# Kernel optimization log

Hardware: AMD Instinct MI355X
Metric: run time of the kernel (lower is better)

The kernel has to match this reference:

```python
import jax, jax.numpy as jnp
import numpy as np

N_NODES = 100000
N_EDGES = 1_000_000
NODE_DIM = 64
EDGE_DIM = 32
HIDDEN = 64


def _unif(key, shape, fan_in):
    bound = 1.0 / np.sqrt(fan_in)
    return jax.random.uniform(key, shape, jnp.float32, -bound, bound)


def setup_inputs() -> dict:
    key = jax.random.key(0)
    ks = jax.random.split(key, 11)
    node_features = jax.random.normal(ks[0], (N_NODES, NODE_DIM), jnp.float32)
    edge_index = jax.random.randint(ks[1], (2, N_EDGES), 0, N_NODES, dtype=jnp.int64)
    edge_features = jax.random.normal(ks[2], (N_EDGES, EDGE_DIM), jnp.float32)
    in_dim = 2 * NODE_DIM + EDGE_DIM
    # message MLP: Linear(in_dim, HIDDEN) -> ReLU -> Linear(HIDDEN, HIDDEN)
    W1 = _unif(ks[3], (HIDDEN, in_dim), in_dim)
    b1 = _unif(ks[4], (HIDDEN,), in_dim)
    W2 = _unif(ks[5], (HIDDEN, HIDDEN), HIDDEN)
    b2 = _unif(ks[6], (HIDDEN,), HIDDEN)
    # GRUCell(input=HIDDEN, hidden=NODE_DIM); gates stacked [r; z; n]
    w_ih = _unif(ks[7], (3 * NODE_DIM, HIDDEN), NODE_DIM)
    w_hh = _unif(ks[8], (3 * NODE_DIM, NODE_DIM), NODE_DIM)
    b_ih = _unif(ks[9], (3 * NODE_DIM,), NODE_DIM)
    b_hh = _unif(ks[10], (3 * NODE_DIM,), NODE_DIM)
    return {
        "node_features": node_features,
        "edge_index": edge_index,
        "edge_features": edge_features,
        "W1": W1, "b1": b1, "W2": W2, "b2": b2,
        "w_ih": w_ih, "w_hh": w_hh, "b_ih": b_ih, "b_hh": b_hh,
    }


def reference(node_features, edge_index, edge_features, W1, b1, W2, b2, w_ih, w_hh, b_ih, b_hh):
    src, dst = edge_index[0], edge_index[1]
    # gather endpoints and build message MLP input: [E, 2*node_dim+edge_dim]
    x = jnp.concatenate([node_features[src], node_features[dst], edge_features], axis=-1)
    h = jax.nn.relu(x @ W1.T + b1)
    messages = h @ W2.T + b2  # [E, HIDDEN]
    # scatter-add into per-node aggregates
    agg = jax.ops.segment_sum(messages, dst, num_segments=node_features.shape[0])
    # GRUCell(agg, node_features) with torch gate order [r, z, n]
    gi = agg @ w_ih.T + b_ih
    gh = node_features @ w_hh.T + b_hh
    i_r, i_z, i_n = jnp.split(gi, 3, axis=-1)
    h_r, h_z, h_n = jnp.split(gh, 3, axis=-1)
    r = jax.nn.sigmoid(i_r + h_r)
    z = jax.nn.sigmoid(i_z + h_z)
    n = jnp.tanh(i_n + r * h_n)
    return (1.0 - z) * n + z * node_features
```

## Files before the change

kernel.cpp:

```cpp
#include <hip/hip_runtime.h>
#include <hip/hip_bf16.h>

#define N_NODES 100000
#define N_EDGES 1000000
#define CAP 64
#define OVF_CAP 65536

typedef __bf16 bf16x8 __attribute__((ext_vector_type(8)));
typedef float  f32x4  __attribute__((ext_vector_type(4)));

#define MFMA(a, b, c) __builtin_amdgcn_mfma_f32_16x16x32_bf16((a), (b), (c), 0, 0, 0)

__device__ __forceinline__ float sigmoid_f(float x) { return 1.f / (1.f + __expf(-x)); }
__device__ __forceinline__ float tanh_f(float x) {
    float cx = fminf(fmaxf(x, -30.f), 30.f);
    float e = __expf(-2.f * cx);
    return (1.f - e) / (1.f + e);
}

__global__ __launch_bounds__(256) void pq_kernel(
    const float* __restrict__ nf, const float* __restrict__ W1,
    const float* __restrict__ b1,
    __bf16* __restrict__ Pb, __bf16* __restrict__ Qb)
{
    const int lane = threadIdx.x & 63;
    const int r = lane & 15, g = lane >> 4;

    bf16x8 Bs[4][2], Bd[4][2];
    #pragma unroll
    for (int nt = 0; nt < 4; ++nt)
        #pragma unroll
        for (int kk = 0; kk < 2; ++kk) {
            const float* ws = &W1[(nt * 16 + r) * 160 + kk * 32 + g * 8];
            const float* wd = ws + 64;
            f32x4 s0 = *(const f32x4*)ws, s1 = *(const f32x4*)(ws + 4);
            f32x4 d0 = *(const f32x4*)wd, d1 = *(const f32x4*)(wd + 4);
            #pragma unroll
            for (int j = 0; j < 4; ++j) {
                Bs[nt][kk][j] = (__bf16)s0[j]; Bs[nt][kk][j + 4] = (__bf16)s1[j];
                Bd[nt][kk][j] = (__bf16)d0[j]; Bd[nt][kk][j + 4] = (__bf16)d1[j];
            }
        }
    float b1v[4];
    #pragma unroll
    for (int nt = 0; nt < 4; ++nt) b1v[nt] = b1[nt * 16 + r];

    const int wid = blockIdx.x * (blockDim.x >> 6) + (threadIdx.x >> 6);
    const int nW  = gridDim.x * (blockDim.x >> 6);
    for (int t = wid; t < N_NODES / 16; t += nW) {
        const int base = t * 16;
        bf16x8 A[2];
        #pragma unroll
        for (int kk = 0; kk < 2; ++kk) {
            const float* p = &nf[(size_t)(base + r) * 64 + kk * 32 + g * 8];
            f32x4 v0 = *(const f32x4*)p, v1 = *(const f32x4*)(p + 4);
            #pragma unroll
            for (int j = 0; j < 4; ++j) { A[kk][j] = (__bf16)v0[j]; A[kk][j + 4] = (__bf16)v1[j]; }
        }
        f32x4 accP[4] = {}, accQ[4] = {};
        #pragma unroll
        for (int nt = 0; nt < 4; ++nt)
            #pragma unroll
            for (int kk = 0; kk < 2; ++kk) {
                accP[nt] = MFMA(A[kk], Bs[nt][kk], accP[nt]);
                accQ[nt] = MFMA(A[kk], Bd[nt][kk], accQ[nt]);
            }
        #pragma unroll
        for (int nt = 0; nt < 4; ++nt)
            #pragma unroll
            for (int rr = 0; rr < 4; ++rr) {
                const int node = base + g * 4 + rr;
                const int col  = nt * 16 + r;
                Pb[(size_t)node * 64 + col] = (__bf16)(accP[nt][rr] + b1v[nt]);
                Qb[(size_t)node * 64 + col] = (__bf16)accQ[nt][rr];
            }
    }
}

__global__ __launch_bounds__(256) void e_kernel(
    const float* __restrict__ ef, const float* __restrict__ W1,
    __bf16* __restrict__ Eb)
{
    const int lane = threadIdx.x & 63;
    const int r = lane & 15, g = lane >> 4;

    bf16x8 Be[4];
    #pragma unroll
    for (int nt = 0; nt < 4; ++nt) {
        const float* w = &W1[(nt * 16 + r) * 160 + 128 + g * 8];
        f32x4 w0 = *(const f32x4*)w, w1 = *(const f32x4*)(w + 4);
        #pragma unroll
        for (int j = 0; j < 4; ++j) { Be[nt][j] = (__bf16)w0[j]; Be[nt][j + 4] = (__bf16)w1[j]; }
    }

    const int wid = blockIdx.x * (blockDim.x >> 6) + (threadIdx.x >> 6);
    const int nW  = gridDim.x * (blockDim.x >> 6);
    for (int t = wid; t < N_EDGES / 16; t += nW) {
        const int base = t * 16;
        bf16x8 Ae;
        {
            const float* p = &ef[(size_t)(base + r) * 32 + g * 8];
            f32x4 v0 = *(const f32x4*)p, v1 = *(const f32x4*)(p + 4);
            #pragma unroll
            for (int j = 0; j < 4; ++j) { Ae[j] = (__bf16)v0[j]; Ae[j + 4] = (__bf16)v1[j]; }
        }
        f32x4 accT[4] = {};
        #pragma unroll
        for (int nt = 0; nt < 4; ++nt) accT[nt] = MFMA(Ae, Be[nt], accT[nt]);
        #pragma unroll
        for (int nt = 0; nt < 4; ++nt)
            #pragma unroll
            for (int rr = 0; rr < 4; ++rr)
                Eb[(size_t)(base + g * 4 + rr) * 64 + nt * 16 + r] = (__bf16)accT[nt][rr];
    }
}

__global__ __launch_bounds__(256) void scatter_kernel(
    const int* __restrict__ ei, int* __restrict__ cnt,
    int2* __restrict__ slots, int* __restrict__ ovf)
{
    const int* srcI = ei;
    const int* dstI = ei + N_EDGES;
    int* ovfCnt = cnt + N_NODES;
    for (int e = blockIdx.x * blockDim.x + threadIdx.x; e < N_EDGES;
         e += gridDim.x * blockDim.x) {
        int d = dstI[e];
        int r = atomicAdd(&cnt[d], 1);
        if (r < CAP) slots[(size_t)d * CAP + r] = make_int2(e, srcI[e]);
        else { int o = atomicAdd(ovfCnt, 1); if (o < OVF_CAP) ovf[o] = e; }
    }
}

__global__ __launch_bounds__(256) void gather_kernel(
    const int* __restrict__ cnt, const int2* __restrict__ slots,
    const __bf16* __restrict__ Eb, const __bf16* __restrict__ Pb,
    const __bf16* __restrict__ Qb, float* __restrict__ Hsum)
{
    const int lane = threadIdx.x & 63;
    const int wid = blockIdx.x * (blockDim.x >> 6) + (threadIdx.x >> 6);
    const int nW  = gridDim.x * (blockDim.x >> 6);
    for (int n = wid; n < N_NODES; n += nW) {
        const int c = cnt[n];
        const int m = min(c, CAP);
        int2 sl = slots[(size_t)n * CAP + lane];
        float q = (float)Qb[(size_t)n * 64 + lane];
        float acc = 0.f;
        float ev = 0.f, pv = 0.f;
        if (m > 0) {
            int e0 = __shfl(sl.x, 0), s0 = __shfl(sl.y, 0);
            ev = (float)Eb[(size_t)e0 * 64 + lane];
            pv = (float)Pb[(size_t)s0 * 64 + lane];
        }
        for (int it = 0; it < m; ++it) {
            float ce = ev, cp = pv;
            if (it + 1 < m) {
                int e1 = __shfl(sl.x, it + 1), s1 = __shfl(sl.y, it + 1);
                ev = (float)Eb[(size_t)e1 * 64 + lane];
                pv = (float)Pb[(size_t)s1 * 64 + lane];
            }
            acc += fmaxf(ce + cp + q, 0.f);
        }
        Hsum[(size_t)n * 64 + lane] = acc;
    }
}

__global__ void ovf_kernel(
    const int* __restrict__ cnt, const int* __restrict__ ovf,
    const int* __restrict__ ei,
    const __bf16* __restrict__ Eb, const __bf16* __restrict__ Pb,
    const __bf16* __restrict__ Qb, float* __restrict__ Hsum)
{
    const int lane = threadIdx.x;
    int nv = min(cnt[N_NODES], OVF_CAP);
    const int* srcI = ei;
    const int* dstI = ei + N_EDGES;
    for (int i = blockIdx.x; i < nv; i += gridDim.x) {
        int e = ovf[i];
        int d = dstI[e], s = srcI[e];
        float v = fmaxf((float)Eb[(size_t)e * 64 + lane] +
                        (float)Pb[(size_t)s * 64 + lane] +
                        (float)Qb[(size_t)d * 64 + lane], 0.f);
        atomicAdd(&Hsum[(size_t)d * 64 + lane], v);
    }
}

__global__ __launch_bounds__(256) void prep_kernel(
    const float* __restrict__ w_ih, const float* __restrict__ W2,
    const float* __restrict__ b2, float* __restrict__ M, float* __restrict__ b2i)
{
    int tid = blockIdx.x * blockDim.x + threadIdx.x;
    if (tid < 192 * 64) {
        int d = tid >> 6, k = tid & 63;
        float s = 0.f;
        #pragma unroll 8
        for (int j = 0; j < 64; ++j) s += w_ih[d * 64 + j] * W2[j * 64 + k];
        M[tid] = s;
    }
    if (tid < 192) {
        float s = 0.f;
        for (int j = 0; j < 64; ++j) s += w_ih[tid * 64 + j] * b2[j];
        b2i[tid] = s;
    }
}

__global__ __launch_bounds__(256) void gru_kernel(
    const float* __restrict__ nf, const float* __restrict__ Hsum,
    const float* __restrict__ M, const float* __restrict__ w_hh,
    const float* __restrict__ b_ih, const float* __restrict__ b_hh,
    const float* __restrict__ b2i, const int* __restrict__ cnt,
    float* __restrict__ out)
{
    const int lane = threadIdx.x & 63;
    const int r = lane & 15, g = lane >> 4;
    const int wid = blockIdx.x * (blockDim.x >> 6) + (threadIdx.x >> 6);
    const int nW  = gridDim.x * (blockDim.x >> 6);

    float br[4], bz[4], bin_[4], bhn_[4];
    float c2r[4], c2z[4], c2n[4];
    #pragma unroll
    for (int nt = 0; nt < 4; ++nt) {
        const int d = nt * 16 + r;
        br[nt]   = b_ih[d] + b_hh[d];
        bz[nt]   = b_ih[64 + d] + b_hh[64 + d];
        bin_[nt] = b_ih[128 + d];
        bhn_[nt] = b_hh[128 + d];
        c2r[nt] = b2i ? b2i[d] : 0.f;
        c2z[nt] = b2i ? b2i[64 + d] : 0.f;
        c2n[nt] = b2i ? b2i[128 + d] : 0.f;
    }

    for (int t = wid; t < N_NODES / 16; t += nW) {
        const int base = t * 16;
        bf16x8 aaH[2], aaL[2], ahH[2], ahL[2];
        #pragma unroll
        for (int kk = 0; kk < 2; ++kk) {
            const float* pa = &Hsum[(size_t)(base + r) * 64 + kk * 32 + g * 8];
            const float* ph = &nf  [(size_t)(base + r) * 64 + kk * 32 + g * 8];
            f32x4 a0 = *(const f32x4*)pa, a1 = *(const f32x4*)(pa + 4);
            f32x4 h0 = *(const f32x4*)ph, h1 = *(const f32x4*)(ph + 4);
            #pragma unroll
            for (int j = 0; j < 4; ++j) {
                float av0 = a0[j], av1 = a1[j], hv0 = h0[j], hv1 = h1[j];
                __bf16 x;
                x = (__bf16)av0; aaH[kk][j]     = x; aaL[kk][j]     = (__bf16)(av0 - (float)x);
                x = (__bf16)av1; aaH[kk][j + 4] = x; aaL[kk][j + 4] = (__bf16)(av1 - (float)x);
                x = (__bf16)hv0; ahH[kk][j]     = x; ahL[kk][j]     = (__bf16)(hv0 - (float)x);
                x = (__bf16)hv1; ahH[kk][j + 4] = x; ahL[kk][j + 4] = (__bf16)(hv1 - (float)x);
            }
        }

        f32x4 accR[4] = {}, accZ[4] = {}, accIN[4] = {}, accHN[4] = {};
        #pragma unroll
        for (int c = 0; c < 3; ++c) {
            bf16x8 Bi[4][2], Bh[4][2];
            #pragma unroll
            for (int nt = 0; nt < 4; ++nt)
                #pragma unroll
                for (int kk = 0; kk < 2; ++kk) {
                    const float* wi = &M   [(size_t)(c * 64 + nt * 16 + r) * 64 + kk * 32 + g * 8];
                    const float* wh = &w_hh[(size_t)(c * 64 + nt * 16 + r) * 64 + kk * 32 + g * 8];
                    f32x4 i0 = *(const f32x4*)wi, i1 = *(const f32x4*)(wi + 4);
                    f32x4 h0 = *(const f32x4*)wh, h1 = *(const f32x4*)(wh + 4);
                    #pragma unroll
                    for (int j = 0; j < 4; ++j) {
                        Bi[nt][kk][j] = (__bf16)i0[j]; Bi[nt][kk][j + 4] = (__bf16)i1[j];
                        Bh[nt][kk][j] = (__bf16)h0[j]; Bh[nt][kk][j + 4] = (__bf16)h1[j];
                    }
                }
            #pragma unroll
            for (int nt = 0; nt < 4; ++nt) {
                f32x4 ai = {}, ah = {};
                #pragma unroll
                for (int kk = 0; kk < 2; ++kk) {
                    ai = MFMA(aaH[kk], Bi[nt][kk], ai);
                    ai = MFMA(aaL[kk], Bi[nt][kk], ai);
                    ah = MFMA(ahH[kk], Bh[nt][kk], ah);
                    ah = MFMA(ahL[kk], Bh[nt][kk], ah);
                }
                if (c == 0)      accR[nt] = ai + ah;
                else if (c == 1) accZ[nt] = ai + ah;
                else             { accIN[nt] = ai; accHN[nt] = ah; }
            }
        }
        #pragma unroll
        for (int nt = 0; nt < 4; ++nt)
            #pragma unroll
            for (int rr = 0; rr < 4; ++rr) {
                const int node = base + g * 4 + rr;
                const int d    = nt * 16 + r;
                float dg = cnt ? (float)cnt[node] : 0.f;
                float rg = sigmoid_f(accR[nt][rr] + br[nt] + dg * c2r[nt]);
                float zg = sigmoid_f(accZ[nt][rr] + bz[nt] + dg * c2z[nt]);
                float ng = tanh_f(accIN[nt][rr] + bin_[nt] + dg * c2n[nt] +
                                  rg * (accHN[nt][rr] + bhn_[nt]));
                float hv = nf[(size_t)node * 64 + d];
                out[(size_t)node * 64 + d] = (1.f - zg) * ng + zg * hv;
            }
    }
}

#define LDH 68
__global__ __launch_bounds__(256) void edge_kernel_fb(
    const int* __restrict__ ei, const float* __restrict__ ef,
    const float* __restrict__ W1, const float* __restrict__ W2,
    const float* __restrict__ b2,
    const __bf16* __restrict__ Pb, const __bf16* __restrict__ Qb,
    float* __restrict__ agg)
{
    __shared__ float lds_h[4][16 * LDH];
    const int lane = threadIdx.x & 63;
    const int r = lane & 15, g = lane >> 4;
    float* hb = lds_h[threadIdx.x >> 6];
    const int* srcI = ei;
    const int* dstI = ei + N_EDGES;

    bf16x8 Be[4];
    #pragma unroll
    for (int nt = 0; nt < 4; ++nt) {
        const float* w = &W1[(nt * 16 + r) * 160 + 128 + g * 8];
        f32x4 w0 = *(const f32x4*)w, w1 = *(const f32x4*)(w + 4);
        #pragma unroll
        for (int j = 0; j < 4; ++j) { Be[nt][j] = (__bf16)w0[j]; Be[nt][j + 4] = (__bf16)w1[j]; }
    }
    bf16x8 B2[4][2];
    #pragma unroll
    for (int nt = 0; nt < 4; ++nt)
        #pragma unroll
        for (int kk = 0; kk < 2; ++kk) {
            const float* w = &W2[(nt * 16 + r) * 64 + kk * 32 + g * 8];
            f32x4 w0 = *(const f32x4*)w, w1 = *(const f32x4*)(w + 4);
            #pragma unroll
            for (int j = 0; j < 4; ++j) { B2[nt][kk][j] = (__bf16)w0[j]; B2[nt][kk][j + 4] = (__bf16)w1[j]; }
        }
    float b2v[4];
    #pragma unroll
    for (int nt = 0; nt < 4; ++nt) b2v[nt] = b2[nt * 16 + r];

    const int wid = blockIdx.x * (blockDim.x >> 6) + (threadIdx.x >> 6);
    const int nW  = gridDim.x * (blockDim.x >> 6);
    for (int t = wid; t < N_EDGES / 16; t += nW) {
        const int base = t * 16;
        const int er = base + r;
        const int es = srcI[er], ed = dstI[er];
        bf16x8 Ae;
        {
            const float* p = &ef[(size_t)er * 32 + g * 8];
            f32x4 v0 = *(const f32x4*)p, v1 = *(const f32x4*)(p + 4);
            #pragma unroll
            for (int j = 0; j < 4; ++j) { Ae[j] = (__bf16)v0[j]; Ae[j + 4] = (__bf16)v1[j]; }
        }
        f32x4 accT[4] = {};
        #pragma unroll
        for (int nt = 0; nt < 4; ++nt) accT[nt] = MFMA(Ae, Be[nt], accT[nt]);
        #pragma unroll
        for (int nt = 0; nt < 4; ++nt)
            #pragma unroll
            for (int rr = 0; rr < 4; ++rr)
                hb[(g * 4 + rr) * LDH + nt * 16 + r] = accT[nt][rr];
        bf16x8 A2[2];
        #pragma unroll
        for (int kk = 0; kk < 2; ++kk) {
            const int k = kk * 32 + g * 8;
            const float* hp = &hb[r * LDH + k];
            f32x4 h0 = *(const f32x4*)hp, h1 = *(const f32x4*)(hp + 4);
            bf16x8 p8 = *(const bf16x8*)(Pb + (size_t)es * 64 + k);
            bf16x8 q8 = *(const bf16x8*)(Qb + (size_t)ed * 64 + k);
            #pragma unroll
            for (int j = 0; j < 4; ++j) {
                A2[kk][j]     = (__bf16)fmaxf(h0[j] + (float)p8[j]     + (float)q8[j],     0.f);
                A2[kk][j + 4] = (__bf16)fmaxf(h1[j] + (float)p8[j + 4] + (float)q8[j + 4], 0.f);
            }
        }
        f32x4 accM[4] = {};
        #pragma unroll
        for (int nt = 0; nt < 4; ++nt)
            #pragma unroll
            for (int kk = 0; kk < 2; ++kk)
                accM[nt] = MFMA(A2[kk], B2[nt][kk], accM[nt]);
        int4 d4 = *(const int4*)(dstI + base + g * 4);
        const int* dd = (const int*)&d4;
        #pragma unroll
        for (int rr = 0; rr < 4; ++rr) {
            float* dp = agg + (size_t)dd[rr] * 64;
            #pragma unroll
            for (int nt = 0; nt < 4; ++nt)
                atomicAdd(dp + nt * 16 + r, accM[nt][rr] + b2v[nt]);
        }
    }
}

extern "C" void kernel_launch(void* const* d_in, const int* in_sizes, int n_in,
                              void* d_out, int out_size, void* d_ws, size_t ws_size,
                              hipStream_t stream) {
    const float* nf  = (const float*)d_in[0];
    const int*   ei  = (const int*)  d_in[1];
    const float* ef  = (const float*)d_in[2];
    const float* W1  = (const float*)d_in[3];
    const float* b1  = (const float*)d_in[4];
    const float* W2  = (const float*)d_in[5];
    const float* b2  = (const float*)d_in[6];
    const float* wih = (const float*)d_in[7];
    const float* whh = (const float*)d_in[8];
    const float* bih = (const float*)d_in[9];
    const float* bhh = (const float*)d_in[10];
    float* out = (float*)d_out;

    char* ws = (char*)d_ws;
    size_t off = 0;
    auto alloc = [&](size_t bytes) { char* p = ws + off; off = (off + bytes + 255) & ~(size_t)255; return p; };
    int*    cnt   = (int*)   alloc((size_t)(N_NODES + 1) * 4);
    int*    ovf   = (int*)   alloc((size_t)OVF_CAP * 4);
    int2*   slots = (int2*)  alloc((size_t)N_NODES * CAP * 8);
    __bf16* Eb    = (__bf16*)alloc((size_t)N_EDGES * 64 * 2);
    __bf16* Pb    = (__bf16*)alloc((size_t)N_NODES * 64 * 2);
    __bf16* Qb    = (__bf16*)alloc((size_t)N_NODES * 64 * 2);
    float*  Hsum  = (float*) alloc((size_t)N_NODES * 64 * 4);
    float*  M     = (float*) alloc((size_t)192 * 64 * 4);
    float*  b2i   = (float*) alloc((size_t)192 * 4);
    const size_t need = off;

    if (ws_size >= need) {
        hipMemsetAsync(cnt, 0, (size_t)(N_NODES + 1) * 4, stream);
        pq_kernel     <<<1563, 256, 0, stream>>>(nf, W1, b1, Pb, Qb);
        e_kernel      <<<2048, 256, 0, stream>>>(ef, W1, Eb);
        scatter_kernel<<<2048, 256, 0, stream>>>(ei, cnt, slots, ovf);
        prep_kernel   <<<48,   256, 0, stream>>>(wih, W2, b2, M, b2i);
        gather_kernel <<<25000, 256, 0, stream>>>(cnt, slots, Eb, Pb, Qb, Hsum);
        ovf_kernel    <<<16,   64,  0, stream>>>(cnt, ovf, ei, Eb, Pb, Qb, Hsum);
        gru_kernel    <<<1563, 256, 0, stream>>>(nf, Hsum, M, whh, bih, bhh, b2i, cnt, out);
    } else {
        float*  agg = (float*)ws;
        __bf16* Pf  = (__bf16*)(ws + (size_t)N_NODES * 64 * 4);
        __bf16* Qf  = (__bf16*)(ws + (size_t)N_NODES * 64 * 4 + (size_t)N_NODES * 64 * 2);
        hipMemsetAsync(agg, 0, (size_t)N_NODES * 64 * 4, stream);
        pq_kernel     <<<1563, 256, 0, stream>>>(nf, W1, b1, Pf, Qf);
        edge_kernel_fb<<<2048, 256, 0, stream>>>(ei, ef, W1, W2, b2, Pf, Qf, agg);
        gru_kernel    <<<1563, 256, 0, stream>>>(nf, agg, wih, whh, bih, bhh, nullptr, nullptr, out);
    }
}
```

Before: 616.2 us.

## Replace fixed-capacity slot buckets with CSR via histogram and prefix scan

Builds a CSR edge layout through a histogram, a three-stage prefix scan and a scatter, replacing the fixed 64-slot-per-node buckets and the overflow path. The edge kernel then writes each edge's projection directly into its CSR position, so the gather reads Eb rows contiguously and batches 8 loads at a time. This removes the 51MB sparse slots array and the overflow atomics, but adds several small kernels, a second pass of atomics, and scattered row writes in e_kernel. Separately, the GRU kernel stages the M and w_hh weights in LDS as swizzled bf16 once per block instead of reloading and converting them from global memory for every tile.

Result: faster. 575.6 us (-6.6%).

```diff
diff --git a/kernel.cpp b/kernel.cpp
--- a/kernel.cpp
+++ b/kernel.cpp
@@ -3,8 +3,8 @@
 
 #define N_NODES 100000
 #define N_EDGES 1000000
-#define CAP 64
-#define OVF_CAP 65536
+#define SCAN_CHUNK 1024
+#define N_SCAN_BLKS ((N_NODES + SCAN_CHUNK - 1) / SCAN_CHUNK)
 
 typedef __bf16 bf16x8 __attribute__((ext_vector_type(8)));
 typedef float  f32x4  __attribute__((ext_vector_type(4)));
@@ -77,9 +77,102 @@
     }
 }
 
+__global__ __launch_bounds__(256) void hist_kernel(
+    const int* __restrict__ ei, int* __restrict__ cnt)
+{
+    const int* dstI = ei + N_EDGES;
+    for (int e = blockIdx.x * blockDim.x + threadIdx.x; e < N_EDGES;
+         e += gridDim.x * blockDim.x)
+        atomicAdd(&cnt[dstI[e]], 1);
+}
+
+__global__ __launch_bounds__(256) void scanA_kernel(
+    const int* __restrict__ cnt, int* __restrict__ blkSum)
+{
+    const int lane = threadIdx.x & 63, w = threadIdx.x >> 6;
+    int base = blockIdx.x * SCAN_CHUNK + threadIdx.x * 4;
+    int s = 0;
+    #pragma unroll
+    for (int j = 0; j < 4; ++j) if (base + j < N_NODES) s += cnt[base + j];
+    #pragma unroll
+    for (int o = 32; o > 0; o >>= 1) s += __shfl_down(s, o);
+    __shared__ int wt[4];
+    if (lane == 0) wt[w] = s;
+    __syncthreads();
+    if (threadIdx.x == 0) blkSum[blockIdx.x] = wt[0] + wt[1] + wt[2] + wt[3];
+}
+
+__global__ void scanB_kernel(int* __restrict__ blkSum)
+{
+    const int lane = threadIdx.x;
+    int carry = 0;
+    for (int c = 0; c < N_SCAN_BLKS; c += 64) {
+        int v = (c + lane < N_SCAN_BLKS) ? blkSum[c + lane] : 0;
+        int inc = v;
+        #pragma unroll
+        for (int o = 1; o < 64; o <<= 1) {
+            int t = __shfl_up(inc, o);
+            if (lane >= o) inc += t;
+        }
+        int ex = inc - v;
+        if (c + lane < N_SCAN_BLKS) blkSum[c + lane] = carry + ex;
+        carry += __shfl(inc, 63);
+    }
+}
+
+__global__ __launch_bounds__(256) void scanC_kernel(
+    const int* __restrict__ cnt, const int* __restrict__ blkSum,
+    int* __restrict__ off, int* __restrict__ cur)
+{
+    const int lane = threadIdx.x & 63, w = threadIdx.x >> 6;
+    int base = blockIdx.x * SCAN_CHUNK + threadIdx.x * 4;
+    int v[4];
+    int tsum = 0;
+    #pragma unroll
+    for (int j = 0; j < 4; ++j) {
+        v[j] = (base + j < N_NODES) ? cnt[base + j] : 0;
+        tsum += v[j];
+    }
+    int inc = tsum;
+    #pragma unroll
+    for (int o = 1; o < 64; o <<= 1) {
+        int t = __shfl_up(inc, o);
+        if (lane >= o) inc += t;
+    }
+    __shared__ int wt[4];
+    if (lane == 63) wt[w] = inc;
+    __syncthreads();
+    int woff = 0;
+    for (int k = 0; k < w; ++k) woff += wt[k];
+    int running = blkSum[blockIdx.x] + woff + inc - tsum;
+    #pragma unroll
+    for (int j = 0; j < 4; ++j) {
+        if (base + j < N_NODES) {
+            off[base + j] = running;
+            cur[base + j] = running;
+            if (base + j == N_NODES - 1) off[N_NODES] = running + v[j];
+            running += v[j];
+        }
+    }
+}
+
+__global__ __launch_bounds__(256) void scatter_kernel(
+    const int* __restrict__ ei, int* __restrict__ cur,
+    int* __restrict__ slotSrc, int* __restrict__ posA)
+{
+    const int* srcI = ei;
+    const int* dstI = ei + N_EDGES;
+    for (int e = blockIdx.x * blockDim.x + threadIdx.x; e < N_EDGES;
+         e += gridDim.x * blockDim.x) {
+        int p = atomicAdd(&cur[dstI[e]], 1);
+        slotSrc[p] = srcI[e];
+        posA[e] = p;
+    }
+}
+
 __global__ __launch_bounds__(256) void e_kernel(
     const float* __restrict__ ef, const float* __restrict__ W1,
-    __bf16* __restrict__ Eb)
+    const int* __restrict__ posA, __bf16* __restrict__ Eb)
 {
     const int lane = threadIdx.x & 63;
     const int r = lane & 15, g = lane >> 4;
@@ -107,32 +200,21 @@
         f32x4 accT[4] = {};
         #pragma unroll
         for (int nt = 0; nt < 4; ++nt) accT[nt] = MFMA(Ae, Be[nt], accT[nt]);
-        #pragma unroll
-        for (int nt = 0; nt < 4; ++nt)
-            #pragma unroll
-            for (int rr = 0; rr < 4; ++rr)
-                Eb[(size_t)(base + g * 4 + rr) * 64 + nt * 16 + r] = (__bf16)accT[nt][rr];
-    }
-}
-
-__global__ __launch_bounds__(256) void scatter_kernel(
-    const int* __restrict__ ei, int* __restrict__ cnt,
-    int2* __restrict__ slots, int* __restrict__ ovf)
-{
-    const int* srcI = ei;
-    const int* dstI = ei + N_EDGES;
-    int* ovfCnt = cnt + N_NODES;
-    for (int e = blockIdx.x * blockDim.x + threadIdx.x; e < N_EDGES;
-         e += gridDim.x * blockDim.x) {
-        int d = dstI[e];
-        int r = atomicAdd(&cnt[d], 1);
-        if (r < CAP) slots[(size_t)d * CAP + r] = make_int2(e, srcI[e]);
-        else { int o = atomicAdd(ovfCnt, 1); if (o < OVF_CAP) ovf[o] = e; }
+
+        int4 p4 = *(const int4*)(posA + base + g * 4);
+        const int* pp = (const int*)&p4;
+        #pragma unroll
+        for (int rr = 0; rr < 4; ++rr) {
+            __bf16* row = Eb + (size_t)pp[rr] * 64;
+            #pragma unroll
+            for (int nt = 0; nt < 4; ++nt)
+                row[nt * 16 + r] = (__bf16)accT[nt][rr];
+        }
     }
 }
 
 __global__ __launch_bounds__(256) void gather_kernel(
-    const int* __restrict__ cnt, const int2* __restrict__ slots,
+    const int* __restrict__ off, const int* __restrict__ slotSrc,
     const __bf16* __restrict__ Eb, const __bf16* __restrict__ Pb,
     const __bf16* __restrict__ Qb, float* __restrict__ Hsum)
 {
@@ -140,47 +222,31 @@
     const int wid = blockIdx.x * (blockDim.x >> 6) + (threadIdx.x >> 6);
     const int nW  = gridDim.x * (blockDim.x >> 6);
     for (int n = wid; n < N_NODES; n += nW) {
-        const int c = cnt[n];
-        const int m = min(c, CAP);
-        int2 sl = slots[(size_t)n * CAP + lane];
+        const int o0 = off[n], o1 = off[n + 1];
+        const int m = o1 - o0;
         float q = (float)Qb[(size_t)n * 64 + lane];
         float acc = 0.f;
-        float ev = 0.f, pv = 0.f;
-        if (m > 0) {
-            int e0 = __shfl(sl.x, 0), s0 = __shfl(sl.y, 0);
-            ev = (float)Eb[(size_t)e0 * 64 + lane];
-            pv = (float)Pb[(size_t)s0 * 64 + lane];
-        }
-        for (int it = 0; it < m; ++it) {
-            float ce = ev, cp = pv;
-            if (it + 1 < m) {
-                int e1 = __shfl(sl.x, it + 1), s1 = __shfl(sl.y, it + 1);
-                ev = (float)Eb[(size_t)e1 * 64 + lane];
-                pv = (float)Pb[(size_t)s1 * 64 + lane];
-            }
-            acc += fmaxf(ce + cp + q, 0.f);
+        int sl = (lane < m) ? slotSrc[o0 + lane] : 0;
+        int i = 0;
+        for (; i + 8 <= m && i + 8 <= 64; i += 8) {
+            float pv[8], evv[8];
+            #pragma unroll
+            for (int j = 0; j < 8; ++j) {
+                int s = __shfl(sl, i + j);
+                pv[j]  = (float)Pb[(size_t)s * 64 + lane];
+                evv[j] = (float)Eb[(size_t)(o0 + i + j) * 64 + lane];
+            }
+            #pragma unroll
+            for (int j = 0; j < 8; ++j)
+                acc += fmaxf(pv[j] + evv[j] + q, 0.f);
+        }
+        for (; i < m; ++i) {
+            int s = (i < 64) ? __shfl(sl, i) : slotSrc[o0 + i];
+            float pv = (float)Pb[(size_t)s * 64 + lane];
+            float ev = (float)Eb[(size_t)(o0 + i) * 64 + lane];
+            acc += fmaxf(pv + ev + q, 0.f);
         }
         Hsum[(size_t)n * 64 + lane] = acc;
-    }
-}
-
-__global__ void ovf_kernel(
-    const int* __restrict__ cnt, const int* __restrict__ ovf,
-    const int* __restrict__ ei,
-    const __bf16* __restrict__ Eb, const __bf16* __restrict__ Pb,
-    const __bf16* __restrict__ Qb, float* __restrict__ Hsum)
-{
-    const int lane = threadIdx.x;
-    int nv = min(cnt[N_NODES], OVF_CAP);
-    const int* srcI = ei;
-    const int* dstI = ei + N_EDGES;
-    for (int i = blockIdx.x; i < nv; i += gridDim.x) {
-        int e = ovf[i];
-        int d = dstI[e], s = srcI[e];
-        float v = fmaxf((float)Eb[(size_t)e * 64 + lane] +
-                        (float)Pb[(size_t)s * 64 + lane] +
-                        (float)Qb[(size_t)d * 64 + lane], 0.f);
-        atomicAdd(&Hsum[(size_t)d * 64 + lane], v);
     }
 }
 
@@ -210,13 +276,27 @@
     const float* __restrict__ b2i, const int* __restrict__ cnt,
     float* __restrict__ out)
 {
+    __shared__ __bf16 w_lds[2 * 192 * 64];
+    for (int ch = threadIdx.x; ch < 3072; ch += 256) {
+        int mat = ch >> 11;
+        mat = ch / 1536;
+        int rr  = (ch - mat * 1536) >> 3;
+        int cc  = ch & 7;
+        const float* sp = (mat == 0 ? M : w_hh) + rr * 64 + cc * 8;
+        f32x4 a = *(const f32x4*)sp, b = *(const f32x4*)(sp + 4);
+        bf16x8 v;
+        #pragma unroll
+        for (int j = 0; j < 4; ++j) { v[j] = (__bf16)a[j]; v[j + 4] = (__bf16)b[j]; }
+        *(bf16x8*)&w_lds[((mat * 192 + rr) * 64) + ((cc ^ (rr & 7)) * 8)] = v;
+    }
+    __syncthreads();
+
     const int lane = threadIdx.x & 63;
     const int r = lane & 15, g = lane >> 4;
     const int wid = blockIdx.x * (blockDim.x >> 6) + (threadIdx.x >> 6);
     const int nW  = gridDim.x * (blockDim.x >> 6);
 
-    float br[4], bz[4], bin_[4], bhn_[4];
-    float c2r[4], c2z[4], c2n[4];
+    float br[4], bz[4], bin_[4], bhn_[4], c2r[4], c2z[4], c2n[4];
     #pragma unroll
     for (int nt = 0; nt < 4; ++nt) {
         const int d = nt * 16 + r;
@@ -228,6 +308,7 @@
         c2z[nt] = b2i ? b2i[64 + d] : 0.f;
         c2n[nt] = b2i ? b2i[128 + d] : 0.f;
     }
+    const int swz = r & 7;
 
     for (int t = wid; t < N_NODES / 16; t += nW) {
         const int base = t * 16;
@@ -251,37 +332,25 @@
 
         f32x4 accR[4] = {}, accZ[4] = {}, accIN[4] = {}, accHN[4] = {};
         #pragma unroll
-        for (int c = 0; c < 3; ++c) {
-            bf16x8 Bi[4][2], Bh[4][2];
-            #pragma unroll
-            for (int nt = 0; nt < 4; ++nt)
-                #pragma unroll
-                for (int kk = 0; kk < 2; ++kk) {
-                    const float* wi = &M   [(size_t)(c * 64 + nt * 16 + r) * 64 + kk * 32 + g * 8];
-                    const float* wh = &w_hh[(size_t)(c * 64 + nt * 16 + r) * 64 + kk * 32 + g * 8];
-                    f32x4 i0 = *(const f32x4*)wi, i1 = *(const f32x4*)(wi + 4);
-                    f32x4 h0 = *(const f32x4*)wh, h1 = *(const f32x4*)(wh + 4);
-                    #pragma unroll
-                    for (int j = 0; j < 4; ++j) {
-                        Bi[nt][kk][j] = (__bf16)i0[j]; Bi[nt][kk][j + 4] = (__bf16)i1[j];
-                        Bh[nt][kk][j] = (__bf16)h0[j]; Bh[nt][kk][j + 4] = (__bf16)h1[j];
-                    }
-                }
+        for (int c = 0; c < 3; ++c)
             #pragma unroll
             for (int nt = 0; nt < 4; ++nt) {
+                const int row = c * 64 + nt * 16 + r;
                 f32x4 ai = {}, ah = {};
                 #pragma unroll
                 for (int kk = 0; kk < 2; ++kk) {
-                    ai = MFMA(aaH[kk], Bi[nt][kk], ai);
-                    ai = MFMA(aaL[kk], Bi[nt][kk], ai);
-                    ah = MFMA(ahH[kk], Bh[nt][kk], ah);
-                    ah = MFMA(ahL[kk], Bh[nt][kk], ah);
+                    const int cc = (kk * 4 + g) ^ swz;
+                    bf16x8 Bi = *(const bf16x8*)&w_lds[row * 64 + cc * 8];
+                    bf16x8 Bh = *(const bf16x8*)&w_lds[(192 + row) * 64 + cc * 8];
+                    ai = MFMA(aaH[kk], Bi, ai);
+                    ai = MFMA(aaL[kk], Bi, ai);
+                    ah = MFMA(ahH[kk], Bh, ah);
+                    ah = MFMA(ahL[kk], Bh, ah);
                 }
                 if (c == 0)      accR[nt] = ai + ah;
                 else if (c == 1) accZ[nt] = ai + ah;
                 else             { accIN[nt] = ai; accHN[nt] = ah; }
             }
-        }
         #pragma unroll
         for (int nt = 0; nt < 4; ++nt)
             #pragma unroll
@@ -406,27 +475,33 @@
     float* out = (float*)d_out;
 
     char* ws = (char*)d_ws;
-    size_t off = 0;
-    auto alloc = [&](size_t bytes) { char* p = ws + off; off = (off + bytes + 255) & ~(size_t)255; return p; };
-    int*    cnt   = (int*)   alloc((size_t)(N_NODES + 1) * 4);
-    int*    ovf   = (int*)   alloc((size_t)OVF_CAP * 4);
-    int2*   slots = (int2*)  alloc((size_t)N_NODES * CAP * 8);
-    __bf16* Eb    = (__bf16*)alloc((size_t)N_EDGES * 64 * 2);
-    __bf16* Pb    = (__bf16*)alloc((size_t)N_NODES * 64 * 2);
-    __bf16* Qb    = (__bf16*)alloc((size_t)N_NODES * 64 * 2);
-    float*  Hsum  = (float*) alloc((size_t)N_NODES * 64 * 4);
-    float*  M     = (float*) alloc((size_t)192 * 64 * 4);
-    float*  b2i   = (float*) alloc((size_t)192 * 4);
-    const size_t need = off;
+    size_t off_b = 0;
+    auto alloc = [&](size_t bytes) { char* p = ws + off_b; off_b = (off_b + bytes + 255) & ~(size_t)255; return p; };
+    int*    cnt     = (int*)   alloc((size_t)N_NODES * 4);
+    int*    offA    = (int*)   alloc((size_t)(N_NODES + 1) * 4);
+    int*    cur     = (int*)   alloc((size_t)N_NODES * 4);
+    int*    blkSum  = (int*)   alloc((size_t)N_SCAN_BLKS * 4);
+    int*    posA    = (int*)   alloc((size_t)N_EDGES * 4);
+    int*    slotSrc = (int*)   alloc((size_t)N_EDGES * 4);
+    __bf16* Eb      = (__bf16*)alloc((size_t)N_EDGES * 64 * 2);
+    __bf16* Pb      = (__bf16*)alloc((size_t)N_NODES * 64 * 2);
+    __bf16* Qb      = (__bf16*)alloc((size_t)N_NODES * 64 * 2);
+    float*  Hsum    = (float*) alloc((size_t)N_NODES * 64 * 4);
+    float*  M       = (float*) alloc((size_t)192 * 64 * 4);
+    float*  b2i     = (float*) alloc((size_t)192 * 4);
+    const size_t need = off_b;
 
     if (ws_size >= need) {
-        hipMemsetAsync(cnt, 0, (size_t)(N_NODES + 1) * 4, stream);
+        hipMemsetAsync(cnt, 0, (size_t)N_NODES * 4, stream);
+        hist_kernel   <<<1024, 256, 0, stream>>>(ei, cnt);
+        scanA_kernel  <<<N_SCAN_BLKS, 256, 0, stream>>>(cnt, blkSum);
+        scanB_kernel  <<<1, 64, 0, stream>>>(blkSum);
+        scanC_kernel  <<<N_SCAN_BLKS, 256, 0, stream>>>(cnt, blkSum, offA, cur);
         pq_kernel     <<<1563, 256, 0, stream>>>(nf, W1, b1, Pb, Qb);
-        e_kernel      <<<2048, 256, 0, stream>>>(ef, W1, Eb);
-        scatter_kernel<<<2048, 256, 0, stream>>>(ei, cnt, slots, ovf);
-        prep_kernel   <<<48,   256, 0, stream>>>(wih, W2, b2, M, b2i);
-        gather_kernel <<<25000, 256, 0, stream>>>(cnt, slots, Eb, Pb, Qb, Hsum);
-        ovf_kernel    <<<16,   64,  0, stream>>>(cnt, ovf, ei, Eb, Pb, Qb, Hsum);
+        prep_kernel   <<<48, 256, 0, stream>>>(wih, W2, b2, M, b2i);
+        scatter_kernel<<<1024, 256, 0, stream>>>(ei, cur, slotSrc, posA);
+        e_kernel      <<<2048, 256, 0, stream>>>(ef, W1, posA, Eb);
+        gather_kernel <<<4096, 256, 0, stream>>>(offA, slotSrc, Eb, Pb, Qb, Hsum);
         gru_kernel    <<<1563, 256, 0, stream>>>(nf, Hsum, M, whh, bih, bhh, b2i, cnt, out);
     } else {
         float*  agg = (float*)ws;
```
